# Kernel optimization log

Hardware: AMD Instinct MI355X
Metric: run time of the kernel (lower is better)

The kernel has to match this reference:

```python
import jax, jax.numpy as jnp
import numpy as np

D_MODEL = 1024
N_HEAD = 16
SEQ = 2048
BATCH = 2


def setup_inputs() -> dict:
    key = jax.random.key(0)
    x = jax.random.normal(key, (BATCH, SEQ, D_MODEL), dtype=jnp.float32)
    return {"x": x}


def reference(x) -> jnp.ndarray:
    B, S, D = x.shape
    H = N_HEAD
    hd = D // H
    # split heads: q=k=v=x -> [B, H, S, hd]
    qkv = x.reshape(B, S, H, hd).transpose(0, 2, 1, 3)
    q = k = v = qkv
    # scores [B, H, S, S], scaled by sqrt(head_dim)
    w = jnp.einsum("bhqd,bhkd->bhqk", q, k) / jnp.sqrt(jnp.asarray(hd, x.dtype))
    # causal mask (nd == ns == S here)
    causal = jnp.tril(jnp.ones((S, S), dtype=bool))
    mask_value = jnp.finfo(w.dtype).min
    w = jnp.where(causal[None, None, :, :], w, mask_value)
    w = jax.nn.softmax(w, axis=-1)
    out = jnp.einsum("bhqk,bhkd->bhqd", w, v)
    # merge heads -> [B, S, D]
    return out.transpose(0, 2, 1, 3).reshape(B, S, D)
```

## Files before the change

### kernel.cpp

```cpp
#include <hip/hip_runtime.h>

#define BATCH  2
#define SEQ    2048
#define DMODEL 1024
#define NHEAD  16
#define HD     64
#define BH     (BATCH * NHEAD)

typedef __attribute__((ext_vector_type(8))) short s8v;
typedef __attribute__((ext_vector_type(4))) float f4v;

__device__ inline unsigned short bf16_rne(float f) {
    unsigned u = __builtin_bit_cast(unsigned, f);
    u += 0x7FFFu + ((u >> 16) & 1u);
    return (unsigned short)(u >> 16);
}

__device__ __forceinline__ unsigned pk_bf16(float lo, float hi) {
    return (unsigned)bf16_rne(lo) | ((unsigned)bf16_rne(hi) << 16);
}

__global__ __launch_bounds__(256) void prep_kernel(const float* __restrict__ x,
                                                   unsigned short* __restrict__ xb,
                                                   unsigned short* __restrict__ xbT) {
    __shared__ unsigned short tile[32 * 66];
    const int id = blockIdx.x;
    const int bh = id & (BH - 1);
    const int st = id >> 5;
    const int b = bh >> 4, h = bh & (NHEAD - 1);
    const int s0 = st * 32;
    const int tid = threadIdx.x;
    const int c4 = tid & 15, r16 = tid >> 4;

#pragma unroll
    for (int p = 0; p < 2; ++p) {
        const int sl = p * 16 + r16;
        const size_t off = (size_t)(b * SEQ + s0 + sl) * DMODEL + h * HD + c4 * 4;
        float4 v = *(const float4*)(x + off);
        ushort4 o;
        o.x = bf16_rne(v.x); o.y = bf16_rne(v.y);
        o.z = bf16_rne(v.z); o.w = bf16_rne(v.w);
        *(ushort4*)(xb + off) = o;
        unsigned short* t = tile + sl * 66 + c4 * 4;
        t[0] = o.x; t[1] = o.y; t[2] = o.z; t[3] = o.w;
    }
    __syncthreads();
    {
        const int d = tid >> 2;
        const int sb = (tid & 3) * 8;
        s8v o;
#pragma unroll
        for (int j = 0; j < 8; ++j)
            o[j] = (short)tile[(sb + j) * 66 + d];
        *(s8v*)(xbT + (size_t)(bh * HD + d) * SEQ + s0 + sb) = o;
    }
}

__device__ __forceinline__ void stage_tile(const unsigned short* __restrict__ xbh,
                                           const unsigned short* __restrict__ xTh,
                                           char* lds, int bufoff, int k0,
                                           int w, int sr, int sc) {
    if (w < 2) {
#pragma unroll
        for (int i = 0; i < 4; ++i) {
            const int r = w * 32 + i * 8 + sr;
            const unsigned short* gsrc =
                xbh + (size_t)(k0 + r) * DMODEL + ((sc ^ (r & 7)) * 8);
            const int loff = __builtin_amdgcn_readfirstlane(bufoff + (w * 32 + i * 8) * 128);
            __builtin_amdgcn_global_load_lds(
                (const __attribute__((address_space(1))) void*)gsrc,
                (__attribute__((address_space(3))) void*)(lds + loff), 16, 0, 0);
        }
    } else {
#pragma unroll
        for (int i = 0; i < 4; ++i) {
            const int d = (w - 2) * 32 + i * 8 + sr;
            const unsigned short* gsrc =
                xTh + (size_t)d * SEQ + k0 + ((sc ^ (d & 7)) * 8);
            const int loff =
                __builtin_amdgcn_readfirstlane(bufoff + 8192 + ((w - 2) * 32 + i * 8) * 128);
            __builtin_amdgcn_global_load_lds(
                (const __attribute__((address_space(1))) void*)gsrc,
                (__attribute__((address_space(3))) void*)(lds + loff), 16, 0, 0);
        }
    }
}

__global__ __launch_bounds__(256, 4) void flash_kernel(const unsigned short* __restrict__ xb,
                                                       const unsigned short* __restrict__ xbT,
                                                       float* __restrict__ out) {
    __shared__ __align__(16) char lds[40960];

    const int id = blockIdx.x;
    const int bh = id & (BH - 1);
    const int t5 = id >> 5;
    const int rr = t5 >> 3, uu = t5 & 7;
    const int qt = (rr == 0) ? (31 - uu) : (rr == 1) ? (16 + uu)
                 : (rr == 2) ? (15 - uu) : uu;
    const int b = bh >> 4, h = bh & (NHEAD - 1);
    const int tid = threadIdx.x;
    const int w = tid >> 6;
    const int lane = tid & 63;
    const int n = lane & 15;
    const int g = lane >> 4;
    const int qbase = qt * 64;

    const unsigned short* xbh = xb + (size_t)b * SEQ * DMODEL + h * HD;
    const unsigned short* xTh = xbT + (size_t)bh * HD * SEQ;

    const int qrow = qbase + w * 16 + n;
    const s8v qf0 = *(const s8v*)(xbh + (size_t)qrow * DMODEL + g * 8);
    const s8v qf1 = *(const s8v*)(xbh + (size_t)qrow * DMODEL + 32 + g * 8);

    int roff0[4], roff1[4];
#pragma unroll
    for (int t = 0; t < 4; ++t) {
        roff0[t] = (t * 16 + n) * 128 + ((g ^ (n & 7)) * 16);
        roff1[t] = (t * 16 + n) * 128 + (((4 + g) ^ (n & 7)) * 16);
    }

    f4v o0 = {0.f, 0.f, 0.f, 0.f}, o1 = o0, o2 = o0, o3 = o0;
    float lsum = 0.0f;
    char* const Pbase = lds + 32768 + w * 2048;

    char* wrP[4];
#pragma unroll
    for (int t = 0; t < 4; ++t)
        wrP[t] = Pbase + (t >> 1) * 1024 + n * 64 +
                 ((((t & 1) * 2 + (g >> 1)) ^ (n & 3)) * 16) + (g & 1) * 8;
    const char* rdP = Pbase + n * 64 + ((g ^ (n & 3)) * 16);

    const int sr = lane >> 3;
    const int sc = lane & 7;

    stage_tile(xbh, xTh, lds, 0, 0, w, sr, sc);

    for (int kt = 0; kt <= qt; ++kt) {
        char* const buf = lds + ((kt & 1) << 14);
        __syncthreads();
        if (kt < qt)
            stage_tile(xbh, xTh, lds, ((kt & 1) ^ 1) << 14, (kt + 1) * 64, w, sr, sc);

        const bool diag = (kt == qt);
#pragma unroll
        for (int t = 0; t < 4; ++t) {
            const s8v kb0 = *(const s8v*)(buf + roff0[t]);
            const s8v kb1 = *(const s8v*)(buf + roff1[t]);
            f4v c = {0.f, 0.f, 0.f, 0.f};
            __builtin_amdgcn_s_setprio(1);
            c = __builtin_amdgcn_mfma_f32_16x16x32_bf16(kb0, qf0, c, 0, 0, 0);
            c = __builtin_amdgcn_mfma_f32_16x16x32_bf16(kb1, qf1, c, 0, 0, 0);
            __builtin_amdgcn_s_setprio(0);
            float p0, p1, p2, p3;
            {
                p0 = __builtin_amdgcn_exp2f(c[0] * 0.18033688011112042f);
                p1 = __builtin_amdgcn_exp2f(c[1] * 0.18033688011112042f);
                p2 = __builtin_amdgcn_exp2f(c[2] * 0.18033688011112042f);
                p3 = __builtin_amdgcn_exp2f(c[3] * 0.18033688011112042f);
                if (diag) {
                    const int kl = t * 16 + g * 4, ql = w * 16 + n;
                    p0 = (kl + 0 <= ql) ? p0 : 0.0f;
                    p1 = (kl + 1 <= ql) ? p1 : 0.0f;
                    p2 = (kl + 2 <= ql) ? p2 : 0.0f;
                    p3 = (kl + 3 <= ql) ? p3 : 0.0f;
                }
            }
            lsum += (p0 + p1) + (p2 + p3);
            uint2 u;
            u.x = pk_bf16(p0, p1);
            u.y = pk_bf16(p2, p3);
            *(uint2*)(wrP[t]) = u;
        }

        const s8v pa0 = *(const s8v*)(rdP);
        const s8v pa1 = *(const s8v*)(rdP + 1024);
        const char* kColB = buf + 8192;
        {
            s8v vb;
            __builtin_amdgcn_s_setprio(1);
            vb = *(const s8v*)(kColB + roff0[0]);
            o0 = __builtin_amdgcn_mfma_f32_16x16x32_bf16(pa0, vb, o0, 0, 0, 0);
            vb = *(const s8v*)(kColB + roff1[0]);
            o0 = __builtin_amdgcn_mfma_f32_16x16x32_bf16(pa1, vb, o0, 0, 0, 0);
            vb = *(const s8v*)(kColB + roff0[1]);
            o1 = __builtin_amdgcn_mfma_f32_16x16x32_bf16(pa0, vb, o1, 0, 0, 0);
            vb = *(const s8v*)(kColB + roff1[1]);
            o1 = __builtin_amdgcn_mfma_f32_16x16x32_bf16(pa1, vb, o1, 0, 0, 0);
            vb = *(const s8v*)(kColB + roff0[2]);
            o2 = __builtin_amdgcn_mfma_f32_16x16x32_bf16(pa0, vb, o2, 0, 0, 0);
            vb = *(const s8v*)(kColB + roff1[2]);
            o2 = __builtin_amdgcn_mfma_f32_16x16x32_bf16(pa1, vb, o2, 0, 0, 0);
            vb = *(const s8v*)(kColB + roff0[3]);
            o3 = __builtin_amdgcn_mfma_f32_16x16x32_bf16(pa0, vb, o3, 0, 0, 0);
            vb = *(const s8v*)(kColB + roff1[3]);
            o3 = __builtin_amdgcn_mfma_f32_16x16x32_bf16(pa1, vb, o3, 0, 0, 0);
            __builtin_amdgcn_s_setprio(0);
        }
    }

    lsum += __shfl_xor(lsum, 16, 64);
    lsum += __shfl_xor(lsum, 32, 64);
    f4v inv;
#pragma unroll
    for (int r = 0; r < 4; ++r)
        inv[r] = 1.0f / __shfl(lsum, g * 4 + r, 64);

    float* outh = out + (size_t)b * SEQ * DMODEL + h * HD;
#pragma unroll
    for (int r = 0; r < 4; ++r) {
        const size_t rowoff = (size_t)(qbase + w * 16 + g * 4 + r) * DMODEL;
        outh[rowoff + 0 * 16 + n] = o0[r] * inv[r];
        outh[rowoff + 1 * 16 + n] = o1[r] * inv[r];
        outh[rowoff + 2 * 16 + n] = o2[r] * inv[r];
        outh[rowoff + 3 * 16 + n] = o3[r] * inv[r];
    }
}

#define KT 32
#define QR 16
#define LDS_STRIDE 68

__global__ __launch_bounds__(64, 2)
void attn_fp32_kernel(const float* __restrict__ x, float* __restrict__ out) {
    __shared__ float kv[KT * LDS_STRIDE];
    const int id = blockIdx.x;
    const int bh = id & (BATCH * NHEAD - 1);
    const int qt = (SEQ / QR - 1) - (id >> 5);
    const int b = bh >> 4, h = bh & (NHEAD - 1);
    const int lane = threadIdx.x;
    const int row = lane & (QR - 1);
    const int slice = lane >> 4;
    const int qrow = qt * QR + row;
    const float* xh = x + (size_t)b * SEQ * DMODEL + (size_t)h * HD;
    float q[HD], o[HD];
    const float4* qp = (const float4*)(xh + (size_t)qrow * DMODEL);
#pragma unroll
    for (int i = 0; i < HD / 4; ++i) {
        float4 v = qp[i];
        q[4*i+0] = v.x * 0.125f; q[4*i+1] = v.y * 0.125f;
        q[4*i+2] = v.z * 0.125f; q[4*i+3] = v.w * 0.125f;
    }
#pragma unroll
    for (int d = 0; d < HD; ++d) o[d] = 0.0f;
    float l = 0.0f;
    const int kend = qt * QR + QR;
    for (int kt0 = 0; kt0 < kend; kt0 += KT) {
        __syncthreads();
#pragma unroll
        for (int i = 0; i < (KT * HD / 4) / 64; ++i) {
            int idx = i * 64 + lane;
            int r = idx >> 4, c = idx & 15;
            *(float4*)(kv + r * LDS_STRIDE + c * 4) =
                *(const float4*)(xh + (size_t)(kt0 + r) * DMODEL + c * 4);
        }
        __syncthreads();
#pragma unroll 2
        for (int jj = 0; jj < KT / 4; ++jj) {
            const int j = jj * 4 + slice;
            const float* kr = kv + j * LDS_STRIDE;
            float a0 = 0.f, a1 = 0.f, a2 = 0.f, a3 = 0.f;
#pragma unroll
            for (int dq = 0; dq < 16; ++dq) {
                float4 kk = ((const float4*)kr)[dq];
                a0 = fmaf(q[4*dq+0], kk.x, a0); a1 = fmaf(q[4*dq+1], kk.y, a1);
                a2 = fmaf(q[4*dq+2], kk.z, a2); a3 = fmaf(q[4*dq+3], kk.w, a3);
            }
            float p = __expf((a0 + a1) + (a2 + a3));
            p = (kt0 + j <= qrow) ? p : 0.0f;
            l += p;
#pragma unroll
            for (int dq = 0; dq < 16; ++dq) {
                float4 vv = ((const float4*)kr)[dq];
                o[4*dq+0] = fmaf(p, vv.x, o[4*dq+0]); o[4*dq+1] = fmaf(p, vv.y, o[4*dq+1]);
                o[4*dq+2] = fmaf(p, vv.z, o[4*dq+2]); o[4*dq+3] = fmaf(p, vv.w, o[4*dq+3]);
            }
        }
    }
    l += __shfl_xor(l, 16, 64);
    l += __shfl_xor(l, 32, 64);
#pragma unroll
    for (int d = 0; d < HD; ++d) {
        o[d] += __shfl_xor(o[d], 16, 64);
        o[d] += __shfl_xor(o[d], 32, 64);
    }
    if (slice == 0) {
        const float invl = 1.0f / l;
        float4* op = (float4*)(out + ((size_t)b * SEQ + qrow) * DMODEL + (size_t)h * HD);
#pragma unroll
        for (int i = 0; i < HD / 4; ++i) {
            float4 v;
            v.x = o[4*i+0] * invl; v.y = o[4*i+1] * invl;
            v.z = o[4*i+2] * invl; v.w = o[4*i+3] * invl;
            op[i] = v;
        }
    }
}

extern "C" void kernel_launch(void* const* d_in, const int* in_sizes, int n_in,
                              void* d_out, int out_size, void* d_ws, size_t ws_size,
                              hipStream_t stream) {
    const float* x = (const float*)d_in[0];
    float* out = (float*)d_out;
    const size_t need = (size_t)2 * BATCH * SEQ * DMODEL * 2;
    if (ws_size >= need) {
        unsigned short* xb  = (unsigned short*)d_ws;
        unsigned short* xbT = xb + (size_t)BATCH * SEQ * DMODEL;
        hipLaunchKernelGGL(prep_kernel, dim3(BH * SEQ / 32), dim3(256), 0, stream, x, xb, xbT);
        hipLaunchKernelGGL(flash_kernel, dim3(BH * SEQ / 64), dim3(256), 0, stream, xb, xbT, out);
    } else {
        hipLaunchKernelGGL(attn_fp32_kernel, dim3(BATCH * NHEAD * (SEQ / QR)), dim3(64), 0,
                           stream, x, out);
    }
}
```

Baseline: 106.5 us.

## Split long causal query tiles across two blocks and combine partial results

Query tiles 16..31 now have their key range split at tile 16 into two blocks that write unnormalized partial outputs and row sums to workspace. A new combine kernel adds the halves and normalizes. The grid grows from 32 to 48 blocks per head and all blocks do about 16-17 key tiles, which shortens the critical path and evens out the load. The cost is an extra kernel launch, partial-output traffic through global memory, and more workspace. Merging by plain addition assumes the scores need no max subtraction, same as before.

```diff
diff --git a/kernel.cpp b/kernel.cpp
--- a/kernel.cpp
+++ b/kernel.cpp
@@ -88,15 +88,24 @@
 
 __global__ __launch_bounds__(256, 4) void flash_kernel(const unsigned short* __restrict__ xb,
                                                        const unsigned short* __restrict__ xbT,
-                                                       float* __restrict__ out) {
+                                                       float* __restrict__ out,
+                                                       float* __restrict__ oPart,
+                                                       float* __restrict__ lPart) {
     __shared__ __align__(16) char lds[40960];
 
     const int id = blockIdx.x;
     const int bh = id & (BH - 1);
-    const int t5 = id >> 5;
-    const int rr = t5 >> 3, uu = t5 & 7;
-    const int qt = (rr == 0) ? (31 - uu) : (rr == 1) ? (16 + uu)
-                 : (rr == 2) ? (15 - uu) : uu;
+    const int j = id >> 5;
+    int qt, kt0, ktEnd, half;
+    bool partial;
+    if (j < 16) {
+        qt = 16 + j; kt0 = 0; ktEnd = 15; partial = true; half = 0;
+    } else {
+        const int r = j - 16;
+        const int L = 16 - (r >> 1);
+        if (r & 1) { qt = L + 15; kt0 = 16; ktEnd = qt; partial = true;  half = 1; }
+        else       { qt = L - 1;  kt0 = 0;  ktEnd = qt; partial = false; half = 0; }
+    }
     const int b = bh >> 4, h = bh & (NHEAD - 1);
     const int tid = threadIdx.x;
     const int w = tid >> 6;
@@ -133,12 +142,12 @@
     const int sr = lane >> 3;
     const int sc = lane & 7;
 
-    stage_tile(xbh, xTh, lds, 0, 0, w, sr, sc);
-
-    for (int kt = 0; kt <= qt; ++kt) {
+    stage_tile(xbh, xTh, lds, 0, kt0 * 64, w, sr, sc);
+
+    for (int kt = kt0; kt <= ktEnd; ++kt) {
         char* const buf = lds + ((kt & 1) << 14);
         __syncthreads();
-        if (kt < qt)
+        if (kt < ktEnd)
             stage_tile(xbh, xTh, lds, ((kt & 1) ^ 1) << 14, (kt + 1) * 64, w, sr, sc);
 
         const bool diag = (kt == qt);
@@ -200,19 +209,62 @@
 
     lsum += __shfl_xor(lsum, 16, 64);
     lsum += __shfl_xor(lsum, 32, 64);
-    f4v inv;
-#pragma unroll
-    for (int r = 0; r < 4; ++r)
-        inv[r] = 1.0f / __shfl(lsum, g * 4 + r, 64);
-
-    float* outh = out + (size_t)b * SEQ * DMODEL + h * HD;
-#pragma unroll
-    for (int r = 0; r < 4; ++r) {
-        const size_t rowoff = (size_t)(qbase + w * 16 + g * 4 + r) * DMODEL;
-        outh[rowoff + 0 * 16 + n] = o0[r] * inv[r];
-        outh[rowoff + 1 * 16 + n] = o1[r] * inv[r];
-        outh[rowoff + 2 * 16 + n] = o2[r] * inv[r];
-        outh[rowoff + 3 * 16 + n] = o3[r] * inv[r];
+
+    if (!partial) {
+        f4v inv;
+#pragma unroll
+        for (int r = 0; r < 4; ++r)
+            inv[r] = 1.0f / __shfl(lsum, g * 4 + r, 64);
+        float* outh = out + (size_t)b * SEQ * DMODEL + h * HD;
+#pragma unroll
+        for (int r = 0; r < 4; ++r) {
+            const size_t rowoff = (size_t)(qbase + w * 16 + g * 4 + r) * DMODEL;
+            outh[rowoff + 0 * 16 + n] = o0[r] * inv[r];
+            outh[rowoff + 1 * 16 + n] = o1[r] * inv[r];
+            outh[rowoff + 2 * 16 + n] = o2[r] * inv[r];
+            outh[rowoff + 3 * 16 + n] = o3[r] * inv[r];
+        }
+    } else {
+        const int slot = (bh * 16 + (qt - 16)) * 2 + half;
+        float* ob = oPart + (size_t)slot * 4096;
+#pragma unroll
+        for (int r = 0; r < 4; ++r) {
+            const int row = w * 16 + g * 4 + r;
+            ob[row * 64 + 0 * 16 + n] = o0[r];
+            ob[row * 64 + 1 * 16 + n] = o1[r];
+            ob[row * 64 + 2 * 16 + n] = o2[r];
+            ob[row * 64 + 3 * 16 + n] = o3[r];
+        }
+        if (g == 0) lPart[slot * 64 + w * 16 + n] = lsum;
+    }
+}
+
+__global__ __launch_bounds__(256) void combine_kernel(const float* __restrict__ oPart,
+                                                      const float* __restrict__ lPart,
+                                                      float* __restrict__ out) {
+    const int bid = blockIdx.x;
+    const int bh = bid & (BH - 1);
+    const int t = bid >> 5;
+    const int b = bh >> 4, h = bh & (NHEAD - 1);
+    const int tid = threadIdx.x;
+    const int row = tid >> 2;
+    const int dq = (tid & 3) * 16;
+    const int slot = (bh * 16 + t) * 2;
+    const float l = lPart[slot * 64 + row] + lPart[(slot + 1) * 64 + row];
+    const float inv = 1.0f / l;
+    const float* lo = oPart + (size_t)slot * 4096 + row * 64 + dq;
+    const float* hi = lo + 4096;
+    float* op = out + ((size_t)(b * SEQ + (16 + t) * 64 + row)) * DMODEL + h * HD + dq;
+#pragma unroll
+    for (int i = 0; i < 4; ++i) {
+        float4 a = *(const float4*)(lo + i * 4);
+        float4 c = *(const float4*)(hi + i * 4);
+        float4 o;
+        o.x = (a.x + c.x) * inv;
+        o.y = (a.y + c.y) * inv;
+        o.z = (a.z + c.z) * inv;
+        o.w = (a.w + c.w) * inv;
+        *(float4*)(op + i * 4) = o;
     }
 }
 
@@ -301,12 +353,21 @@
                               hipStream_t stream) {
     const float* x = (const float*)d_in[0];
     float* out = (float*)d_out;
-    const size_t need = (size_t)2 * BATCH * SEQ * DMODEL * 2;
+    const size_t nXb = (size_t)BATCH * SEQ * DMODEL;
+    const size_t nOP = (size_t)BH * 16 * 2 * 4096;
+    const size_t nLP = (size_t)BH * 16 * 2 * 64;
+    const size_t need = 2 * nXb * 2 + (nOP + nLP) * 4;
     if (ws_size >= need) {
         unsigned short* xb  = (unsigned short*)d_ws;
-        unsigned short* xbT = xb + (size_t)BATCH * SEQ * DMODEL;
-        hipLaunchKernelGGL(prep_kernel, dim3(BH * SEQ / 32), dim3(256), 0, stream, x, xb, xbT);
-        hipLaunchKernelGGL(flash_kernel, dim3(BH * SEQ / 64), dim3(256), 0, stream, xb, xbT, out);
+        unsigned short* xbT = xb + nXb;
+        float* oPart = (float*)(xbT + nXb);
+        float* lPart = oPart + nOP;
+        hipLaunchKernelGGL(prep_kernel, dim3(BH * SEQ / 32), dim3(256), 0, stream,
+                           x, xb, xbT);
+        hipLaunchKernelGGL(flash_kernel, dim3(BH * 48), dim3(256), 0, stream,
+                           xb, xbT, out, oPart, lPart);
+        hipLaunchKernelGGL(combine_kernel, dim3(BH * 16), dim3(256), 0, stream,
+                           oPart, lPart, out);
     } else {
         hipLaunchKernelGGL(attn_fp32_kernel, dim3(BATCH * NHEAD * (SEQ / QR)), dim3(64), 0,
                            stream, x, out);
```

New measurement: 113.1 us. +6.2%, slower.
